# Optimization experiments

Measured on AMD Instinct MI355X. Metric: run time of the kernel, lower is better.

## Reference

```python
import jax, jax.numpy as jnp
import numpy as np

D_HIDDEN = 1024
D_MODEL = 1024
R_MIN, R_MAX = 0.0, 1.0
MAX_PHASE = 6.28
SEQ_LEN = 16384


def setup_inputs() -> dict:
    key = jax.random.key(0)
    k_in, k_th, k_nu, k_bre, k_bim, k_cre, k_cim, k_d = jax.random.split(key, 8)
    inputs = jax.random.normal(k_in, (SEQ_LEN, D_MODEL), dtype=jnp.float32)
    # theta_log ~ log(max_phase * U)
    u_th = jax.random.uniform(k_th, (D_HIDDEN,), dtype=jnp.float32)
    theta_log = jnp.log(MAX_PHASE * u_th)
    # nu_log ~ log(-0.5 * log(U*(r_max^2 - r_min^2) + r_min^2))
    u_nu = jax.random.uniform(k_nu, (D_HIDDEN,), dtype=jnp.float32)
    nu_log = jnp.log(-0.5 * jnp.log(u_nu * (R_MAX**2 - R_MIN**2) + R_MIN**2))
    # gamma_log = log(sqrt(1 - |lambda|^2))
    diag_lambda = jnp.exp(-jnp.exp(nu_log) + 1j * jnp.exp(theta_log))
    gamma_log = jnp.log(jnp.sqrt(1.0 - jnp.abs(diag_lambda) ** 2))
    norm_b = jnp.sqrt(2.0 * D_MODEL)
    norm_c = jnp.sqrt(1.0 * D_HIDDEN)
    B_re = jax.random.normal(k_bre, (D_HIDDEN, D_MODEL), dtype=jnp.float32) / norm_b
    B_im = jax.random.normal(k_bim, (D_HIDDEN, D_MODEL), dtype=jnp.float32) / norm_b
    C_re = jax.random.normal(k_cre, (D_MODEL, D_HIDDEN), dtype=jnp.float32) / norm_c
    C_im = jax.random.normal(k_cim, (D_MODEL, D_HIDDEN), dtype=jnp.float32) / norm_c
    Dp = jax.random.normal(k_d, (D_MODEL,), dtype=jnp.float32)
    return {"inputs": inputs, "nu_log": nu_log, "theta_log": theta_log,
            "gamma_log": gamma_log, "B_re": B_re, "B_im": B_im,
            "C_re": C_re, "C_im": C_im, "Dp": Dp}


def _binop(q_i, q_j):
    # elementwise associative op for diagonal linear recurrence
    A_i, b_i = q_i
    A_j, b_j = q_j
    return (A_j * A_i, A_j * b_i + b_j)


def reference(inputs, nu_log, theta_log, gamma_log, B_re, B_im, C_re, C_im, Dp):
    # diag_lambda: [H] complex64
    diag_lambda = jnp.exp(-jnp.exp(nu_log) + 1j * jnp.exp(theta_log))
    B_norm = (B_re + 1j * B_im) * jnp.exp(gamma_log)[:, None]  # [H, D]
    C = C_re + 1j * C_im                                        # [D, H]
    L = inputs.shape[0]
    # Bu_t = B_norm @ x_t  -> [L, H] complex
    Bu = inputs.astype(B_norm.dtype) @ B_norm.T
    Lambda = jnp.broadcast_to(diag_lambda[None, :], (L, diag_lambda.shape[0]))
    # parallel scan of h_t = lambda * h_{t-1} + Bu_t (initial state = 0)
    _, hidden = jax.lax.associative_scan(_binop, (Lambda, Bu))  # [L, H]
    # y_t = Re[C h_t] + D * x_t
    outputs = jnp.real(hidden @ C.T) + Dp * inputs              # [L, D]
    return (hidden[-1:], outputs)
```

## Files before the change

kernel.cpp:

```cpp
#include <hip/hip_runtime.h>
#include <stdint.h>
#include <stddef.h>

typedef __bf16 bf16;
typedef __attribute__((ext_vector_type(8))) __bf16 bf16x8;
typedef __attribute__((ext_vector_type(4))) __bf16 bf16x4;
typedef __attribute__((ext_vector_type(2))) __bf16 bf16x2;
typedef __attribute__((ext_vector_type(4))) float f32x4;
typedef __attribute__((ext_vector_type(2))) float f32x2;

#define L_SEQ 16384
#define DH    1024
#define DM    1024
#define NC    256
#define LC    (L_SEQ / NC)

__device__ __forceinline__ void async_copy16(const void* g, void* l) {
  __builtin_amdgcn_global_load_lds((const __attribute__((address_space(1))) void*)g,
                                   (__attribute__((address_space(3))) void*)l,
                                   16, 0, 0);
}


__global__ void k_prep_params(const float* __restrict__ nu_log,
                              const float* __restrict__ theta_log,
                              float* __restrict__ lam_re, float* __restrict__ lam_im,
                              float* __restrict__ lamC_re, float* __restrict__ lamC_im) {
  int h = blockIdx.x * blockDim.x + threadIdx.x;
  if (h >= DH) return;
  float nu  = expf(nu_log[h]);
  float th  = expf(theta_log[h]);
  float mag = expf(-nu);
  float lr = mag * cosf(th);
  float li = mag * sinf(th);
  lam_re[h] = lr; lam_im[h] = li;
  float ar = lr, ai = li;
#pragma unroll
  for (int i = 0; i < 6; ++i) {
    float nr = ar * ar - ai * ai;
    float ni = 2.f * ar * ai;
    ar = nr; ai = ni;
  }
  lamC_re[h] = ar; lamC_im[h] = ai;
}

#define NB_CAST 8192
#define NB_W    1024
__global__ void k_prep_all(const float* __restrict__ x, bf16* __restrict__ xb,
                           const float* __restrict__ B_re, const float* __restrict__ B_im,
                           const float* __restrict__ gamma_log, bf16* __restrict__ Wcat,
                           const float* __restrict__ C_re, const float* __restrict__ C_im,
                           bf16* __restrict__ Ccat) {
  const int b = blockIdx.x;
  if (b < NB_CAST) {
    int i = (b * 256 + (int)threadIdx.x) * 8;
    const float4 a0 = *(const float4*)(x + i);
    const float4 a1 = *(const float4*)(x + i + 4);
    bf16x8 v;
    v[0] = (bf16)a0.x; v[1] = (bf16)a0.y; v[2] = (bf16)a0.z; v[3] = (bf16)a0.w;
    v[4] = (bf16)a1.x; v[5] = (bf16)a1.y; v[6] = (bf16)a1.z; v[7] = (bf16)a1.w;
    *(bf16x8*)(xb + i) = v;
  } else if (b < NB_CAST + NB_W) {
    int idx = ((b - NB_CAST) * 256 + (int)threadIdx.x) * 4;
    int h = idx / DM;
    int d = idx - h * DM;
    float g = expf(gamma_log[h]);
    float4 re = *(const float4*)(B_re + idx);
    float4 im = *(const float4*)(B_im + idx);
    bf16x4 vr, vi;
    vr[0] = (bf16)(re.x * g); vr[1] = (bf16)(re.y * g);
    vr[2] = (bf16)(re.z * g); vr[3] = (bf16)(re.w * g);
    vi[0] = (bf16)(im.x * g); vi[1] = (bf16)(im.y * g);
    vi[2] = (bf16)(im.z * g); vi[3] = (bf16)(im.w * g);
    *(bf16x4*)(Wcat + (size_t)h * DM + d)        = vr;
    *(bf16x4*)(Wcat + (size_t)(DH + h) * DM + d) = vi;
  } else {
    int idx = ((b - NB_CAST - NB_W) * 256 + (int)threadIdx.x) * 4;
    int d = idx / DH;
    int k = idx - d * DH;
    float4 re = *(const float4*)(C_re + idx);
    float4 im = *(const float4*)(C_im + idx);
    bf16x4 vr, vi;
    vr[0] = (bf16)re.x; vr[1] = (bf16)re.y; vr[2] = (bf16)re.z; vr[3] = (bf16)re.w;
    vi[0] = (bf16)(-im.x); vi[1] = (bf16)(-im.y); vi[2] = (bf16)(-im.z); vi[3] = (bf16)(-im.w);
    *(bf16x4*)(Ccat + (size_t)d * (2 * DH) + k)      = vr;
    *(bf16x4*)(Ccat + (size_t)d * (2 * DH) + DH + k) = vi;
  }
}

template <int MODE>
__global__ __launch_bounds__(256, 3)
void k_gemm(const bf16* __restrict__ A, const bf16* __restrict__ B,
            void* __restrict__ Cout, const float* __restrict__ x,
            const float* __restrict__ dp, int K, int N) {
  __shared__ bf16 As[128 * 64];
  __shared__ bf16 Bs[128 * 64];
  const int tid  = threadIdx.x;
  const int lane = tid & 63;
  const int wave = tid >> 6;
  const int wm = wave >> 1, wn = wave & 1;
  const int quad = lane >> 4;
  const int l16  = lane & 15;
  const int m0 = blockIdx.x * 128;
  const int n0 = blockIdx.y * 128;

  f32x4 acc[4][4];
#pragma unroll
  for (int i = 0; i < 4; ++i)
#pragma unroll
    for (int j = 0; j < 4; ++j)
      acc[i][j] = f32x4{0.f, 0.f, 0.f, 0.f};

  for (int k0 = 0; k0 < K; k0 += 64) {
    __syncthreads();
#pragma unroll
    for (int q = 0; q < 4; ++q) {
      const int c = q * 256 + tid;
      const int row = c >> 3, slot = c & 7;
      const int part = slot ^ (row & 7);
      async_copy16(A + (size_t)(m0 + row) * K + k0 + part * 8, (char*)As + c * 16);
      async_copy16(B + (size_t)(n0 + row) * K + k0 + part * 8, (char*)Bs + c * 16);
    }
    __syncthreads();
#pragma unroll
    for (int kk = 0; kk < 64; kk += 32) {
      const int pbase = (kk >> 3);
      bf16x8 fa[4], fb[4];
#pragma unroll
      for (int i = 0; i < 4; ++i) {
        const int ra = wm * 64 + i * 16 + l16;
        const int rb = wn * 64 + i * 16 + l16;
        const int sa = (pbase + quad) ^ (ra & 7);
        const int sb = (pbase + quad) ^ (rb & 7);
        fa[i] = *(const bf16x8*)(As + ra * 64 + sa * 8);
        fb[i] = *(const bf16x8*)(Bs + rb * 64 + sb * 8);
      }
#pragma unroll
      for (int i = 0; i < 4; ++i)
#pragma unroll
        for (int j = 0; j < 4; ++j)
          acc[i][j] = __builtin_amdgcn_mfma_f32_16x16x32_bf16(fa[i], fb[j], acc[i][j], 0, 0, 0);
    }
  }

  const int crow0 = m0 + wm * 64 + quad * 4;
  const int ccol0 = n0 + wn * 64 + l16;
  if (MODE == 0) {
    bf16* out = (bf16*)Cout;
#pragma unroll
    for (int i = 0; i < 4; ++i)
#pragma unroll
      for (int j = 0; j < 4; ++j)
#pragma unroll
        for (int p = 0; p < 4; ++p)
          out[(size_t)(crow0 + i * 16 + p) * N + ccol0 + j * 16] = (bf16)acc[i][j][p];
  } else {
    float* out = (float*)Cout;
#pragma unroll
    for (int j = 0; j < 4; ++j) {
      const int col = ccol0 + j * 16;
      const float dpv = dp[col];
#pragma unroll
      for (int i = 0; i < 4; ++i)
#pragma unroll
        for (int p = 0; p < 4; ++p) {
          const int row = crow0 + i * 16 + p;
          out[(size_t)row * N + col] = acc[i][j][p] + dpv * x[(size_t)row * N + col];
        }
    }
  }
}


__global__ void k_scan_local(const bf16* __restrict__ Bu,
                             const float* __restrict__ lam_re,
                             const float* __restrict__ lam_im,
                             float* __restrict__ chunk_end) {
  const int h2 = (blockIdx.y * 256 + threadIdx.x) * 2;
  const int c = blockIdx.x;
  const float lr0 = lam_re[h2],     li0 = lam_im[h2];
  const float lr1 = lam_re[h2 + 1], li1 = lam_im[h2 + 1];
  float hr0 = 0.f, hi0 = 0.f, hr1 = 0.f, hi1 = 0.f;
  const bf16* p = Bu + (size_t)c * LC * (2 * DH) + h2;
#pragma unroll 4
  for (int t = 0; t < LC; ++t) {
    bf16x2 br = *(const bf16x2*)(p);
    bf16x2 bi = *(const bf16x2*)(p + DH);
    float nr0 = lr0 * hr0 - li0 * hi0 + (float)br[0];
    float ni0 = lr0 * hi0 + li0 * hr0 + (float)bi[0];
    float nr1 = lr1 * hr1 - li1 * hi1 + (float)br[1];
    float ni1 = lr1 * hi1 + li1 * hr1 + (float)bi[1];
    hr0 = nr0; hi0 = ni0; hr1 = nr1; hi1 = ni1;
    p += 2 * DH;
  }
  *(f32x4*)(chunk_end + (size_t)c * (2 * DH) + 2 * h2) = f32x4{hr0, hi0, hr1, hi1};
}

__global__ void k_scan_chunks(const float* __restrict__ chunk_end,
                              const float* __restrict__ lamC_re,
                              const float* __restrict__ lamC_im,
                              float* __restrict__ carry_in,
                              float* __restrict__ out_final,
                              int interleave) {
  const int h = blockIdx.x * 256 + threadIdx.x;
  const float lr = lamC_re[h], li = lamC_im[h];
  float er = 0.f, ei = 0.f;
#pragma unroll 16
  for (int c = 0; c < NC; ++c) {
    *(f32x2*)(carry_in + (size_t)c * (2 * DH) + 2 * h) = f32x2{er, ei};
    f32x2 ce = *(const f32x2*)(chunk_end + (size_t)c * (2 * DH) + 2 * h);
    float nr = lr * er - li * ei + ce[0];
    float ni = lr * ei + li * er + ce[1];
    er = nr; ei = ni;
  }
  if (interleave) {
    out_final[2 * h]     = er;
    out_final[2 * h + 1] = ei;
  } else {
    out_final[h] = er;
  }
}

__global__ void k_scan_apply(bf16* __restrict__ Bu,
                             const float* __restrict__ lam_re,
                             const float* __restrict__ lam_im,
                             const float* __restrict__ carry_in) {
  const int h2 = (blockIdx.y * 256 + threadIdx.x) * 2;
  const int c = blockIdx.x;
  const float lr0 = lam_re[h2],     li0 = lam_im[h2];
  const float lr1 = lam_re[h2 + 1], li1 = lam_im[h2 + 1];
  f32x4 cv = *(const f32x4*)(carry_in + (size_t)c * (2 * DH) + 2 * h2);
  float hr0 = cv[0], hi0 = cv[1], hr1 = cv[2], hi1 = cv[3];
  bf16* p = Bu + (size_t)c * LC * (2 * DH) + h2;
#pragma unroll 4
  for (int t = 0; t < LC; ++t) {
    bf16x2 br = *(const bf16x2*)(p);
    bf16x2 bi = *(const bf16x2*)(p + DH);
    float nr0 = lr0 * hr0 - li0 * hi0 + (float)br[0];
    float ni0 = lr0 * hi0 + li0 * hr0 + (float)bi[0];
    float nr1 = lr1 * hr1 - li1 * hi1 + (float)br[1];
    float ni1 = lr1 * hi1 + li1 * hr1 + (float)bi[1];
    hr0 = nr0; hi0 = ni0; hr1 = nr1; hi1 = ni1;
    bf16x2 wr, wi;
    wr[0] = (bf16)hr0; wr[1] = (bf16)hr1;
    wi[0] = (bf16)hi0; wi[1] = (bf16)hi1;
    *(bf16x2*)(p)      = wr;
    *(bf16x2*)(p + DH) = wi;
    p += 2 * DH;
  }
}


extern "C" void kernel_launch(void* const* d_in, const int* in_sizes, int n_in,
                              void* d_out, int out_size, void* d_ws, size_t ws_size,
                              hipStream_t stream) {
  const float* inputs    = (const float*)d_in[0];
  const float* nu_log    = (const float*)d_in[1];
  const float* theta_log = (const float*)d_in[2];
  const float* gamma_log = (const float*)d_in[3];
  const float* B_re      = (const float*)d_in[4];
  const float* B_im      = (const float*)d_in[5];
  const float* C_re      = (const float*)d_in[6];
  const float* C_im      = (const float*)d_in[7];
  const float* Dp        = (const float*)d_in[8];

  char* ws = (char*)d_ws;
  float* lam_re    = (float*)(ws + 0);
  float* lam_im    = (float*)(ws + 4096);
  float* lamC_re   = (float*)(ws + 8192);
  float* lamC_im   = (float*)(ws + 12288);
  float* chunk_end = (float*)(ws + 65536);
  float* carry_in  = (float*)(ws + 65536 + (2u << 20));
  bf16*  Wcat      = (bf16*) (ws + 65536 + (4u << 20));
  bf16*  Ccat      = (bf16*) (ws + 65536 + (8u << 20));
  bf16*  Xb        = (bf16*) (ws + 65536 + (12u << 20));
  bf16*  Bu        = (bf16*) (ws + 65536 + (44u << 20));

  int interleave = 1;
  int state_floats = 2048;
  if (out_size == 1024 + L_SEQ * DM) { interleave = 0; state_floats = 1024; }

  float* out_state = (float*)d_out;
  float* out_y     = (float*)d_out + state_floats;

  k_prep_params<<<dim3(4), dim3(256), 0, stream>>>(nu_log, theta_log,
                                                   lam_re, lam_im, lamC_re, lamC_im);
  k_prep_all<<<dim3(NB_CAST + 2 * NB_W), dim3(256), 0, stream>>>(
      inputs, Xb, B_re, B_im, gamma_log, Wcat, C_re, C_im, Ccat);

  k_gemm<0><<<dim3(L_SEQ / 128, (2 * DH) / 128), dim3(256), 0, stream>>>(
      Xb, Wcat, (void*)Bu, nullptr, nullptr, DM, 2 * DH);

  k_scan_local<<<dim3(NC, 2), dim3(256), 0, stream>>>(Bu, lam_re, lam_im, chunk_end);
  k_scan_chunks<<<dim3(4), dim3(256), 0, stream>>>(chunk_end, lamC_re, lamC_im,
                                                   carry_in, out_state, interleave);
  k_scan_apply<<<dim3(NC, 2), dim3(256), 0, stream>>>(Bu, lam_re, lam_im, carry_in);

  k_gemm<1><<<dim3(L_SEQ / 128, DM / 128), dim3(256), 0, stream>>>(
      Bu, Ccat, (void*)out_y, inputs, Dp, 2 * DH, DM);

  (void)in_sizes; (void)n_in; (void)ws_size;
}
```

Before: 396.3 us.

## Fold chunk-carry scan into apply kernel, merge param prep, swizzle GEMM blocks

```diff
diff --git a/kernel.cpp b/kernel.cpp
--- a/kernel.cpp
+++ b/kernel.cpp
@@ -21,36 +21,17 @@
                                    16, 0, 0);
 }
 
-
-__global__ void k_prep_params(const float* __restrict__ nu_log,
-                              const float* __restrict__ theta_log,
-                              float* __restrict__ lam_re, float* __restrict__ lam_im,
-                              float* __restrict__ lamC_re, float* __restrict__ lamC_im) {
-  int h = blockIdx.x * blockDim.x + threadIdx.x;
-  if (h >= DH) return;
-  float nu  = expf(nu_log[h]);
-  float th  = expf(theta_log[h]);
-  float mag = expf(-nu);
-  float lr = mag * cosf(th);
-  float li = mag * sinf(th);
-  lam_re[h] = lr; lam_im[h] = li;
-  float ar = lr, ai = li;
-#pragma unroll
-  for (int i = 0; i < 6; ++i) {
-    float nr = ar * ar - ai * ai;
-    float ni = 2.f * ar * ai;
-    ar = nr; ai = ni;
-  }
-  lamC_re[h] = ar; lamC_im[h] = ai;
-}
-
 #define NB_CAST 8192
 #define NB_W    1024
 __global__ void k_prep_all(const float* __restrict__ x, bf16* __restrict__ xb,
                            const float* __restrict__ B_re, const float* __restrict__ B_im,
                            const float* __restrict__ gamma_log, bf16* __restrict__ Wcat,
                            const float* __restrict__ C_re, const float* __restrict__ C_im,
-                           bf16* __restrict__ Ccat) {
+                           bf16* __restrict__ Ccat,
+                           const float* __restrict__ nu_log,
+                           const float* __restrict__ theta_log,
+                           float* __restrict__ lam_re, float* __restrict__ lam_im,
+                           float* __restrict__ lamC_re, float* __restrict__ lamC_im) {
   const int b = blockIdx.x;
   if (b < NB_CAST) {
     int i = (b * 256 + (int)threadIdx.x) * 8;
@@ -74,7 +55,7 @@
     vi[2] = (bf16)(im.z * g); vi[3] = (bf16)(im.w * g);
     *(bf16x4*)(Wcat + (size_t)h * DM + d)        = vr;
     *(bf16x4*)(Wcat + (size_t)(DH + h) * DM + d) = vi;
-  } else {
+  } else if (b < NB_CAST + 2 * NB_W) {
     int idx = ((b - NB_CAST - NB_W) * 256 + (int)threadIdx.x) * 4;
     int d = idx / DH;
     int k = idx - d * DH;
@@ -85,6 +66,24 @@
     vi[0] = (bf16)(-im.x); vi[1] = (bf16)(-im.y); vi[2] = (bf16)(-im.z); vi[3] = (bf16)(-im.w);
     *(bf16x4*)(Ccat + (size_t)d * (2 * DH) + k)      = vr;
     *(bf16x4*)(Ccat + (size_t)d * (2 * DH) + DH + k) = vi;
+  } else {
+    int h = (b - NB_CAST - 2 * NB_W) * 256 + (int)threadIdx.x;
+    if (h < DH) {
+      float nu  = expf(nu_log[h]);
+      float th  = expf(theta_log[h]);
+      float mag = expf(-nu);
+      float lr = mag * cosf(th);
+      float li = mag * sinf(th);
+      lam_re[h] = lr; lam_im[h] = li;
+      float ar = lr, ai = li;
+#pragma unroll
+      for (int i = 0; i < 6; ++i) {
+        float nr = ar * ar - ai * ai;
+        float ni = 2.f * ar * ai;
+        ar = nr; ai = ni;
+      }
+      lamC_re[h] = ar; lamC_im[h] = ai;
+    }
   }
 }
 
@@ -101,8 +100,16 @@
   const int wm = wave >> 1, wn = wave & 1;
   const int quad = lane >> 4;
   const int l16  = lane & 15;
-  const int m0 = blockIdx.x * 128;
-  const int n0 = blockIdx.y * 128;
+
+  const int lin = blockIdx.y * gridDim.x + blockIdx.x;
+  const int nY  = gridDim.y;
+  const int per = 8 * nY;
+  const int sg  = lin / per;
+  const int r   = lin - sg * per;
+  const int bx  = sg * 8 + (r & 7);
+  const int by  = r >> 3;
+  const int m0 = bx * 128;
+  const int n0 = by * 128;
 
   f32x4 acc[4][4];
 #pragma unroll
@@ -196,41 +203,33 @@
   *(f32x4*)(chunk_end + (size_t)c * (2 * DH) + 2 * h2) = f32x4{hr0, hi0, hr1, hi1};
 }
 
-__global__ void k_scan_chunks(const float* __restrict__ chunk_end,
-                              const float* __restrict__ lamC_re,
-                              const float* __restrict__ lamC_im,
-                              float* __restrict__ carry_in,
-                              float* __restrict__ out_final,
-                              int interleave) {
-  const int h = blockIdx.x * 256 + threadIdx.x;
-  const float lr = lamC_re[h], li = lamC_im[h];
-  float er = 0.f, ei = 0.f;
-#pragma unroll 16
-  for (int c = 0; c < NC; ++c) {
-    *(f32x2*)(carry_in + (size_t)c * (2 * DH) + 2 * h) = f32x2{er, ei};
-    f32x2 ce = *(const f32x2*)(chunk_end + (size_t)c * (2 * DH) + 2 * h);
-    float nr = lr * er - li * ei + ce[0];
-    float ni = lr * ei + li * er + ce[1];
-    er = nr; ei = ni;
-  }
-  if (interleave) {
-    out_final[2 * h]     = er;
-    out_final[2 * h + 1] = ei;
-  } else {
-    out_final[h] = er;
-  }
-}
-
 __global__ void k_scan_apply(bf16* __restrict__ Bu,
                              const float* __restrict__ lam_re,
                              const float* __restrict__ lam_im,
-                             const float* __restrict__ carry_in) {
+                             const float* __restrict__ lamC_re,
+                             const float* __restrict__ lamC_im,
+                             const float* __restrict__ chunk_end,
+                             float* __restrict__ out_final,
+                             int interleave) {
   const int h2 = (blockIdx.y * 256 + threadIdx.x) * 2;
   const int c = blockIdx.x;
   const float lr0 = lam_re[h2],     li0 = lam_im[h2];
   const float lr1 = lam_re[h2 + 1], li1 = lam_im[h2 + 1];
-  f32x4 cv = *(const f32x4*)(carry_in + (size_t)c * (2 * DH) + 2 * h2);
-  float hr0 = cv[0], hi0 = cv[1], hr1 = cv[2], hi1 = cv[3];
+  const float Lr0 = lamC_re[h2],     Li0 = lamC_im[h2];
+  const float Lr1 = lamC_re[h2 + 1], Li1 = lamC_im[h2 + 1];
+
+  float cr0 = 0.f, ci0 = 0.f, cr1 = 0.f, ci1 = 0.f;
+  const float* ce = chunk_end + 2 * h2;
+  for (int j = 0; j < c; ++j) {
+    f32x4 e = *(const f32x4*)(ce + (size_t)j * (2 * DH));
+    float nr0 = Lr0 * cr0 - Li0 * ci0 + e[0];
+    float ni0 = Lr0 * ci0 + Li0 * cr0 + e[1];
+    float nr1 = Lr1 * cr1 - Li1 * ci1 + e[2];
+    float ni1 = Lr1 * ci1 + Li1 * cr1 + e[3];
+    cr0 = nr0; ci0 = ni0; cr1 = nr1; ci1 = ni1;
+  }
+
+  float hr0 = cr0, hi0 = ci0, hr1 = cr1, hi1 = ci1;
   bf16* p = Bu + (size_t)c * LC * (2 * DH) + h2;
 #pragma unroll 4
   for (int t = 0; t < LC; ++t) {
@@ -248,6 +247,16 @@
     *(bf16x2*)(p + DH) = wi;
     p += 2 * DH;
   }
+
+  if (c == NC - 1) {
+    if (interleave) {
+      *(f32x2*)(out_final + 2 * h2)       = f32x2{hr0, hi0};
+      *(f32x2*)(out_final + 2 * (h2 + 1)) = f32x2{hr1, hi1};
+    } else {
+      out_final[h2]     = hr0;
+      out_final[h2 + 1] = hr1;
+    }
+  }
 }
 
 
@@ -270,7 +279,6 @@
   float* lamC_re   = (float*)(ws + 8192);
   float* lamC_im   = (float*)(ws + 12288);
   float* chunk_end = (float*)(ws + 65536);
-  float* carry_in  = (float*)(ws + 65536 + (2u << 20));
   bf16*  Wcat      = (bf16*) (ws + 65536 + (4u << 20));
   bf16*  Ccat      = (bf16*) (ws + 65536 + (8u << 20));
   bf16*  Xb        = (bf16*) (ws + 65536 + (12u << 20));
@@ -283,18 +291,16 @@
   float* out_state = (float*)d_out;
   float* out_y     = (float*)d_out + state_floats;
 
-  k_prep_params<<<dim3(4), dim3(256), 0, stream>>>(nu_log, theta_log,
-                                                   lam_re, lam_im, lamC_re, lamC_im);
-  k_prep_all<<<dim3(NB_CAST + 2 * NB_W), dim3(256), 0, stream>>>(
-      inputs, Xb, B_re, B_im, gamma_log, Wcat, C_re, C_im, Ccat);
+  k_prep_all<<<dim3(NB_CAST + 2 * NB_W + 4), dim3(256), 0, stream>>>(
+      inputs, Xb, B_re, B_im, gamma_log, Wcat, C_re, C_im, Ccat,
+      nu_log, theta_log, lam_re, lam_im, lamC_re, lamC_im);
 
   k_gemm<0><<<dim3(L_SEQ / 128, (2 * DH) / 128), dim3(256), 0, stream>>>(
       Xb, Wcat, (void*)Bu, nullptr, nullptr, DM, 2 * DH);
 
   k_scan_local<<<dim3(NC, 2), dim3(256), 0, stream>>>(Bu, lam_re, lam_im, chunk_end);
-  k_scan_chunks<<<dim3(4), dim3(256), 0, stream>>>(chunk_end, lamC_re, lamC_im,
-                                                   carry_in, out_state, interleave);
-  k_scan_apply<<<dim3(NC, 2), dim3(256), 0, stream>>>(Bu, lam_re, lam_im, carry_in);
+  k_scan_apply<<<dim3(NC, 2), dim3(256), 0, stream>>>(Bu, lam_re, lam_im, lamC_re, lamC_im,
+                                                      chunk_end, out_state, interleave);
 
   k_gemm<1><<<dim3(L_SEQ / 128, DM / 128), dim3(256), 0, stream>>>(
       Bu, Ccat, (void*)out_y, inputs, Dp, 2 * DH, DM);
```

Result: faster. 375.8 us (-5.2%).

## Fuse chunk-local scan into Bu GEMM epilogue with interleaved complex layout

Applied to the files above, without the earlier changes.

```diff
diff --git a/kernel.cpp b/kernel.cpp
--- a/kernel.cpp
+++ b/kernel.cpp
@@ -12,6 +12,7 @@
 #define L_SEQ 16384
 #define DH    1024
 #define DM    1024
+#define NH2   2048
 #define NC    256
 #define LC    (L_SEQ / NC)
 
@@ -21,27 +22,11 @@
                                    16, 0, 0);
 }
 
-
-__global__ void k_prep_params(const float* __restrict__ nu_log,
-                              const float* __restrict__ theta_log,
-                              float* __restrict__ lam_re, float* __restrict__ lam_im,
-                              float* __restrict__ lamC_re, float* __restrict__ lamC_im) {
-  int h = blockIdx.x * blockDim.x + threadIdx.x;
-  if (h >= DH) return;
-  float nu  = expf(nu_log[h]);
-  float th  = expf(theta_log[h]);
-  float mag = expf(-nu);
-  float lr = mag * cosf(th);
-  float li = mag * sinf(th);
-  lam_re[h] = lr; lam_im[h] = li;
-  float ar = lr, ai = li;
-#pragma unroll
-  for (int i = 0; i < 6; ++i) {
-    float nr = ar * ar - ai * ai;
-    float ni = 2.f * ar * ai;
-    ar = nr; ai = ni;
-  }
-  lamC_re[h] = ar; lamC_im[h] = ai;
+__device__ __forceinline__ float bf_lo(uint32_t w) {
+  uint32_t u = w << 16; float f; __builtin_memcpy(&f, &u, 4); return f;
+}
+__device__ __forceinline__ float bf_hi(uint32_t w) {
+  uint32_t u = w & 0xffff0000u; float f; __builtin_memcpy(&f, &u, 4); return f;
 }
 
 #define NB_CAST 8192
@@ -50,7 +35,11 @@
                            const float* __restrict__ B_re, const float* __restrict__ B_im,
                            const float* __restrict__ gamma_log, bf16* __restrict__ Wcat,
                            const float* __restrict__ C_re, const float* __restrict__ C_im,
-                           bf16* __restrict__ Ccat) {
+                           bf16* __restrict__ Ccat,
+                           const float* __restrict__ nu_log,
+                           const float* __restrict__ theta_log,
+                           float* __restrict__ lam_re, float* __restrict__ lam_im,
+                           float* __restrict__ lamC_re, float* __restrict__ lamC_im) {
   const int b = blockIdx.x;
   if (b < NB_CAST) {
     int i = (b * 256 + (int)threadIdx.x) * 8;
@@ -72,19 +61,38 @@
     vr[2] = (bf16)(re.z * g); vr[3] = (bf16)(re.w * g);
     vi[0] = (bf16)(im.x * g); vi[1] = (bf16)(im.y * g);
     vi[2] = (bf16)(im.z * g); vi[3] = (bf16)(im.w * g);
-    *(bf16x4*)(Wcat + (size_t)h * DM + d)        = vr;
-    *(bf16x4*)(Wcat + (size_t)(DH + h) * DM + d) = vi;
-  } else {
+    *(bf16x4*)(Wcat + (size_t)(2 * h) * DM + d)     = vr;
+    *(bf16x4*)(Wcat + (size_t)(2 * h + 1) * DM + d) = vi;
+  } else if (b < NB_CAST + 2 * NB_W) {
     int idx = ((b - NB_CAST - NB_W) * 256 + (int)threadIdx.x) * 4;
     int d = idx / DH;
     int k = idx - d * DH;
     float4 re = *(const float4*)(C_re + idx);
     float4 im = *(const float4*)(C_im + idx);
-    bf16x4 vr, vi;
-    vr[0] = (bf16)re.x; vr[1] = (bf16)re.y; vr[2] = (bf16)re.z; vr[3] = (bf16)re.w;
-    vi[0] = (bf16)(-im.x); vi[1] = (bf16)(-im.y); vi[2] = (bf16)(-im.z); vi[3] = (bf16)(-im.w);
-    *(bf16x4*)(Ccat + (size_t)d * (2 * DH) + k)      = vr;
-    *(bf16x4*)(Ccat + (size_t)d * (2 * DH) + DH + k) = vi;
+    bf16x8 v;
+    v[0] = (bf16)re.x; v[1] = (bf16)(-im.x);
+    v[2] = (bf16)re.y; v[3] = (bf16)(-im.y);
+    v[4] = (bf16)re.z; v[5] = (bf16)(-im.z);
+    v[6] = (bf16)re.w; v[7] = (bf16)(-im.w);
+    *(bf16x8*)(Ccat + (size_t)d * NH2 + 2 * k) = v;
+  } else {
+    int h = (b - NB_CAST - 2 * NB_W) * 256 + (int)threadIdx.x;
+    if (h < DH) {
+      float nu  = expf(nu_log[h]);
+      float th  = expf(theta_log[h]);
+      float mag = expf(-nu);
+      float lr = mag * cosf(th);
+      float li = mag * sinf(th);
+      lam_re[h] = lr; lam_im[h] = li;
+      float ar = lr, ai = li;
+#pragma unroll
+      for (int i = 0; i < 6; ++i) {
+        float nr = ar * ar - ai * ai;
+        float ni = 2.f * ar * ai;
+        ar = nr; ai = ni;
+      }
+      lamC_re[h] = ar; lamC_im[h] = ai;
+    }
   }
 }
 
@@ -92,17 +100,28 @@
 __global__ __launch_bounds__(256, 3)
 void k_gemm(const bf16* __restrict__ A, const bf16* __restrict__ B,
             void* __restrict__ Cout, const float* __restrict__ x,
-            const float* __restrict__ dp, int K, int N) {
-  __shared__ bf16 As[128 * 64];
-  __shared__ bf16 Bs[128 * 64];
+            const float* __restrict__ dp,
+            const float* __restrict__ lam_re, const float* __restrict__ lam_im,
+            float* __restrict__ chunk_end, int K, int N) {
+  __shared__ char smem[32768];
+  bf16* As = (bf16*)smem;
+  bf16* Bs = (bf16*)(smem + 16384);
   const int tid  = threadIdx.x;
   const int lane = tid & 63;
   const int wave = tid >> 6;
   const int wm = wave >> 1, wn = wave & 1;
   const int quad = lane >> 4;
   const int l16  = lane & 15;
-  const int m0 = blockIdx.x * 128;
-  const int n0 = blockIdx.y * 128;
+
+  const int lin = blockIdx.y * gridDim.x + blockIdx.x;
+  const int nY  = gridDim.y;
+  const int per = 8 * nY;
+  const int sg  = lin / per;
+  const int r   = lin - sg * per;
+  const int bx  = sg * 8 + (r & 7);
+  const int by  = r >> 3;
+  const int m0 = bx * 128;
+  const int n0 = by * 128;
 
   f32x4 acc[4][4];
 #pragma unroll
@@ -143,19 +162,56 @@
     }
   }
 
-  const int crow0 = m0 + wm * 64 + quad * 4;
-  const int ccol0 = n0 + wn * 64 + l16;
   if (MODE == 0) {
+    __syncthreads();
+    bf16* T = (bf16*)smem;
+#pragma unroll
+    for (int i = 0; i < 4; ++i)
+#pragma unroll
+      for (int j = 0; j < 4; ++j) {
+        const int col = wn * 64 + j * 16 + l16;
+        const int grp = col >> 3, cin = col & 7;
+#pragma unroll
+        for (int p = 0; p < 4; ++p) {
+          const int row = wm * 64 + i * 16 + quad * 4 + p;
+          T[row * 128 + ((grp ^ (row & 7)) << 3) + cin] = (bf16)acc[i][j][p];
+        }
+      }
+    __syncthreads();
     bf16* out = (bf16*)Cout;
-#pragma unroll
-    for (int i = 0; i < 4; ++i)
-#pragma unroll
-      for (int j = 0; j < 4; ++j)
-#pragma unroll
-        for (int p = 0; p < 4; ++p)
-          out[(size_t)(crow0 + i * 16 + p) * N + ccol0 + j * 16] = (bf16)acc[i][j][p];
+    {
+      const int row = tid >> 1, half = tid & 1;
+#pragma unroll
+      for (int o = 0; o < 8; ++o) {
+        const int grp = half * 8 + o;
+        bf16x8 v = *(const bf16x8*)(T + row * 128 + ((grp ^ (row & 7)) << 3));
+        *(bf16x8*)(out + (size_t)(m0 + row) * N + n0 + grp * 8) = v;
+      }
+    }
+    if (tid < 128) {
+      const int ck = tid >> 6;
+      const int ch = tid & 63;
+      const int gch = (n0 >> 1) + ch;
+      const float lr = lam_re[gch], li = lam_im[gch];
+      float hr = 0.f, hi = 0.f;
+      const int waddr0 = (((ch >> 2) ) << 3) + ((2 * ch) & 7);
+#pragma unroll 8
+      for (int t = 0; t < 64; ++t) {
+        const int row = ck * 64 + t;
+        const int grpsw = ((ch >> 2) ^ (row & 7)) << 3;
+        uint32_t w = *(const uint32_t*)(T + row * 128 + grpsw + ((2 * ch) & 7));
+        float br = bf_lo(w), bi = bf_hi(w);
+        float nr = lr * hr - li * hi + br;
+        float ni = lr * hi + li * hr + bi;
+        hr = nr; hi = ni;
+      }
+      (void)waddr0;
+      *(f32x2*)(chunk_end + (size_t)(2 * bx + ck) * NH2 + n0 + 2 * ch) = f32x2{hr, hi};
+    }
   } else {
     float* out = (float*)Cout;
+    const int crow0 = m0 + wm * 64 + quad * 4;
+    const int ccol0 = n0 + wn * 64 + l16;
 #pragma unroll
     for (int j = 0; j < 4; ++j) {
       const int col = ccol0 + j * 16;
@@ -171,51 +227,25 @@
   }
 }
 
-
-__global__ void k_scan_local(const bf16* __restrict__ Bu,
-                             const float* __restrict__ lam_re,
-                             const float* __restrict__ lam_im,
-                             float* __restrict__ chunk_end) {
-  const int h2 = (blockIdx.y * 256 + threadIdx.x) * 2;
-  const int c = blockIdx.x;
-  const float lr0 = lam_re[h2],     li0 = lam_im[h2];
-  const float lr1 = lam_re[h2 + 1], li1 = lam_im[h2 + 1];
-  float hr0 = 0.f, hi0 = 0.f, hr1 = 0.f, hi1 = 0.f;
-  const bf16* p = Bu + (size_t)c * LC * (2 * DH) + h2;
-#pragma unroll 4
-  for (int t = 0; t < LC; ++t) {
-    bf16x2 br = *(const bf16x2*)(p);
-    bf16x2 bi = *(const bf16x2*)(p + DH);
-    float nr0 = lr0 * hr0 - li0 * hi0 + (float)br[0];
-    float ni0 = lr0 * hi0 + li0 * hr0 + (float)bi[0];
-    float nr1 = lr1 * hr1 - li1 * hi1 + (float)br[1];
-    float ni1 = lr1 * hi1 + li1 * hr1 + (float)bi[1];
-    hr0 = nr0; hi0 = ni0; hr1 = nr1; hi1 = ni1;
-    p += 2 * DH;
-  }
-  *(f32x4*)(chunk_end + (size_t)c * (2 * DH) + 2 * h2) = f32x4{hr0, hi0, hr1, hi1};
-}
-
-__global__ void k_scan_chunks(const float* __restrict__ chunk_end,
-                              const float* __restrict__ lamC_re,
-                              const float* __restrict__ lamC_im,
-                              float* __restrict__ carry_in,
-                              float* __restrict__ out_final,
-                              int interleave) {
+__global__ void k_scan_carry(const float* __restrict__ chunk_end,
+                             const float* __restrict__ lamC_re,
+                             const float* __restrict__ lamC_im,
+                             float* __restrict__ carry_in,
+                             float* __restrict__ out_final,
+                             int interleave) {
   const int h = blockIdx.x * 256 + threadIdx.x;
   const float lr = lamC_re[h], li = lamC_im[h];
   float er = 0.f, ei = 0.f;
 #pragma unroll 16
   for (int c = 0; c < NC; ++c) {
-    *(f32x2*)(carry_in + (size_t)c * (2 * DH) + 2 * h) = f32x2{er, ei};
-    f32x2 ce = *(const f32x2*)(chunk_end + (size_t)c * (2 * DH) + 2 * h);
+    *(f32x2*)(carry_in + (size_t)c * NH2 + 2 * h) = f32x2{er, ei};
+    f32x2 ce = *(const f32x2*)(chunk_end + (size_t)c * NH2 + 2 * h);
     float nr = lr * er - li * ei + ce[0];
     float ni = lr * ei + li * er + ce[1];
     er = nr; ei = ni;
   }
   if (interleave) {
-    out_final[2 * h]     = er;
-    out_final[2 * h + 1] = ei;
+    *(f32x2*)(out_final + 2 * h) = f32x2{er, ei};
   } else {
     out_final[h] = er;
   }
@@ -225,28 +255,27 @@
                              const float* __restrict__ lam_re,
                              const float* __restrict__ lam_im,
                              const float* __restrict__ carry_in) {
-  const int h2 = (blockIdx.y * 256 + threadIdx.x) * 2;
+  const int colbase = (blockIdx.y * 256 + (int)threadIdx.x) * 4;
   const int c = blockIdx.x;
-  const float lr0 = lam_re[h2],     li0 = lam_im[h2];
-  const float lr1 = lam_re[h2 + 1], li1 = lam_im[h2 + 1];
-  f32x4 cv = *(const f32x4*)(carry_in + (size_t)c * (2 * DH) + 2 * h2);
+  const int h0 = colbase >> 1;
+  const float lr0 = lam_re[h0],     li0 = lam_im[h0];
+  const float lr1 = lam_re[h0 + 1], li1 = lam_im[h0 + 1];
+  f32x4 cv = *(const f32x4*)(carry_in + (size_t)c * NH2 + colbase);
   float hr0 = cv[0], hi0 = cv[1], hr1 = cv[2], hi1 = cv[3];
-  bf16* p = Bu + (size_t)c * LC * (2 * DH) + h2;
+  bf16* p = Bu + (size_t)c * LC * NH2 + colbase;
 #pragma unroll 4
   for (int t = 0; t < LC; ++t) {
-    bf16x2 br = *(const bf16x2*)(p);
-    bf16x2 bi = *(const bf16x2*)(p + DH);
-    float nr0 = lr0 * hr0 - li0 * hi0 + (float)br[0];
-    float ni0 = lr0 * hi0 + li0 * hr0 + (float)bi[0];
-    float nr1 = lr1 * hr1 - li1 * hi1 + (float)br[1];
-    float ni1 = lr1 * hi1 + li1 * hr1 + (float)bi[1];
+    bf16x4 b = *(const bf16x4*)(p);
+    float nr0 = lr0 * hr0 - li0 * hi0 + (float)b[0];
+    float ni0 = lr0 * hi0 + li0 * hr0 + (float)b[1];
+    float nr1 = lr1 * hr1 - li1 * hi1 + (float)b[2];
+    float ni1 = lr1 * hi1 + li1 * hr1 + (float)b[3];
     hr0 = nr0; hi0 = ni0; hr1 = nr1; hi1 = ni1;
-    bf16x2 wr, wi;
-    wr[0] = (bf16)hr0; wr[1] = (bf16)hr1;
-    wi[0] = (bf16)hi0; wi[1] = (bf16)hi1;
-    *(bf16x2*)(p)      = wr;
-    *(bf16x2*)(p + DH) = wi;
-    p += 2 * DH;
+    bf16x4 wv;
+    wv[0] = (bf16)hr0; wv[1] = (bf16)hi0;
+    wv[2] = (bf16)hr1; wv[3] = (bf16)hi1;
+    *(bf16x4*)(p) = wv;
+    p += NH2;
   }
 }
 
@@ -283,21 +312,19 @@
   float* out_state = (float*)d_out;
   float* out_y     = (float*)d_out + state_floats;
 
-  k_prep_params<<<dim3(4), dim3(256), 0, stream>>>(nu_log, theta_log,
-                                                   lam_re, lam_im, lamC_re, lamC_im);
-  k_prep_all<<<dim3(NB_CAST + 2 * NB_W), dim3(256), 0, stream>>>(
-      inputs, Xb, B_re, B_im, gamma_log, Wcat, C_re, C_im, Ccat);
-
-  k_gemm<0><<<dim3(L_SEQ / 128, (2 * DH) / 128), dim3(256), 0, stream>>>(
-      Xb, Wcat, (void*)Bu, nullptr, nullptr, DM, 2 * DH);
-
-  k_scan_local<<<dim3(NC, 2), dim3(256), 0, stream>>>(Bu, lam_re, lam_im, chunk_end);
-  k_scan_chunks<<<dim3(4), dim3(256), 0, stream>>>(chunk_end, lamC_re, lamC_im,
-                                                   carry_in, out_state, interleave);
+  k_prep_all<<<dim3(NB_CAST + 2 * NB_W + 4), dim3(256), 0, stream>>>(
+      inputs, Xb, B_re, B_im, gamma_log, Wcat, C_re, C_im, Ccat,
+      nu_log, theta_log, lam_re, lam_im, lamC_re, lamC_im);
+
+  k_gemm<0><<<dim3(L_SEQ / 128, NH2 / 128), dim3(256), 0, stream>>>(
+      Xb, Wcat, (void*)Bu, nullptr, nullptr, lam_re, lam_im, chunk_end, DM, NH2);
+
+  k_scan_carry<<<dim3(4), dim3(256), 0, stream>>>(chunk_end, lamC_re, lamC_im,
+                                                  carry_in, out_state, interleave);
   k_scan_apply<<<dim3(NC, 2), dim3(256), 0, stream>>>(Bu, lam_re, lam_im, carry_in);
 
   k_gemm<1><<<dim3(L_SEQ / 128, DM / 128), dim3(256), 0, stream>>>(
-      Bu, Ccat, (void*)out_y, inputs, Dp, 2 * DH, DM);
+      Bu, Ccat, (void*)out_y, inputs, Dp, nullptr, nullptr, nullptr, NH2, DM);
 
   (void)in_sizes; (void)n_in; (void)ws_size;
 }
```

Measured after the change: 375.7 us. -5.2%, faster.
